# Kernel tuning notes

Hardware: AMD Instinct MI355X
Metric: run time of the kernel (lower is better)

The kernel has to match this reference:

```python
import jax, jax.numpy as jnp
import numpy as np
from jax import lax

N_WIN = 232
T = 8            # timesteps
CHUNK = N_WIN // T  # 29
BETA = 0.9
THR = 1.0
POOL_DIV = 4.0 * 4.0 * 4.0  # avgpool3d kernel volume


@jax.custom_vjp
def spike(x):
    # Heaviside forward (snntorch fire: mem_shift > 0)
    return (x > 0).astype(x.dtype)

def _spike_fwd(x):
    return spike(x), x

def _spike_bwd(x, g):
    # snntorch ATan surrogate, alpha=2: grad = 1 / (1 + (pi*x)^2)
    return (g / (1.0 + (jnp.pi * x) ** 2),)

spike.defvjp(_spike_fwd, _spike_bwd)


def lif(cur, mem, beta, thr):
    # snntorch Leaky, reset_mechanism='subtract': reset uses previous mem
    reset = spike(mem - thr)
    mem_new = beta * mem + cur - reset * thr
    spk = spike(mem_new - thr)
    return spk, mem_new


def setup_inputs() -> dict:
    key = jax.random.key(0)
    ks = jax.random.split(key, 8)
    B, C, H, W = 16, 3, 96, 96
    h0, h1 = 2048, 1024
    input_dim = 47 * 47       # 2209
    in_feat = C * h1 * 13     # 39936
    return {
        "x": jax.random.normal(ks[0], (B, C, N_WIN, H, W), jnp.float32),
        "W_in": jax.random.normal(ks[1], (h0, input_dim), jnp.float32) / np.sqrt(input_dim).astype(np.float32),
        "b_in": jax.random.normal(ks[2], (h0,), jnp.float32) * 0.01,
        "W_hid": jax.random.normal(ks[3], (h1, h0), jnp.float32) / np.sqrt(h0).astype(np.float32),
        "b_hid": jax.random.normal(ks[4], (h1,), jnp.float32) * 0.01,
        "W_out": jax.random.normal(ks[5], (4, in_feat), jnp.float32) / np.sqrt(in_feat).astype(np.float32),
        "b_out": jax.random.normal(ks[6], (4,), jnp.float32) * 0.01,
    }


def reference(x, W_in, b_in, W_hid, b_hid, W_out, b_out):
    B, C, _, H, W = x.shape
    # split time into T chunks of CHUNK, pool each chunk independently
    x6 = x[:, :, : T * CHUNK].reshape(B, C, T, CHUNK, H, W)
    pooled = lax.reduce_window(x6, 0.0, lax.add,
                               (1, 1, 1, 4, 4, 4), (1, 1, 1, 2, 2, 2), "VALID") / POOL_DIV
    Dp, Hp, Wp = pooled.shape[3], pooled.shape[4], pooled.shape[5]  # 13, 47, 47
    # [T, B, C*Dp, Hp*Wp]
    xs = pooled.transpose(2, 0, 1, 3, 4, 5).reshape(T, B, C * Dp, Hp * Wp)
    # fc_in is per-step independent -> precompute for all steps
    cur_in_all = jnp.einsum("tbnf,hf->tbnh", xs, W_in) + b_in

    def step(carry, cur_in):
        m_in, m_hid, m_out = carry
        spk_in, m_in = lif(cur_in, m_in, BETA, THR)
        cur_hid = jnp.einsum("bnh,gh->bng", spk_in, W_hid) + b_hid
        spk_hid, m_hid = lif(cur_hid, m_hid, BETA, THR)
        cur_out = spk_hid.reshape(B, -1) @ W_out.T + b_out
        spk_out, m_out = lif(cur_out, m_out, BETA, 1.0)  # li_out threshold=1.0
        return (m_in, m_hid, m_out), spk_out

    init = (jnp.zeros((B, C * Dp, W_in.shape[0]), x.dtype),
            jnp.zeros((B, C * Dp, W_hid.shape[0]), x.dtype),
            jnp.zeros((B, W_out.shape[0]), x.dtype))
    _, spk_rec = lax.scan(step, init, cur_in_all)
    return spk_rec  # [T, B, n_classes]
```

## Files before the change

### kernel.cpp

```cpp
#include <hip/hip_runtime.h>
#include <hip/hip_bf16.h>

typedef unsigned short ushort_t;
typedef __bf16 bf16x8 __attribute__((ext_vector_type(8)));
typedef float f32x4 __attribute__((ext_vector_type(4)));

#define NROWS 4992
#define KPAD 2240
#define KREAL 2209
#define NH 2048

#define OFF_XS      ((size_t)0)
#define OFF_WINB    ((size_t)22364160)
#define OFF_CURIN   ((size_t)31539200)
#define OFF_CNT1    ((size_t)72433664)
#define OFF_BITS1   ((size_t)72453632)
#define OFF_CNT2    ((size_t)73731584)
#define OFF_BITS2   ((size_t)73732096)
#define ZERO_BYTES  ((size_t)(74371072 - 72433664))
#define OFF_LIST1   ((size_t)74371072)
#define OFF_LIST2   ((size_t)75649024)

#define GLOAD16(g, l) __builtin_amdgcn_global_load_lds( \
    (const __attribute__((address_space(1))) void*)(g), \
    (__attribute__((address_space(3))) void*)(l), 16, 0, 0)

__global__ __launch_bounds__(256) void convert_win(const float* __restrict__ W,
                                                   __hip_bfloat16* __restrict__ Wb) {
    int idx = blockIdx.x * 256 + threadIdx.x;
    int n = idx / KPAD, k = idx - n * KPAD;
    float v = (k < KREAL) ? W[(size_t)n * KREAL + k] : 0.f;
    Wb[idx] = __float2bfloat16(v);
}

__global__ __launch_bounds__(256) void pool_kernel(const float* __restrict__ x,
                                                   __hip_bfloat16* __restrict__ xs) {
    __shared__ float slice[26 * 96];
    __shared__ float acc[2][12 * 47];
    const int tid = threadIdx.x;
    const int band = blockIdx.y;
    const int blk = blockIdx.x;
    const int t = blk & 7;
    const int bc = blk >> 3;
    const int b = bc / 3, c = bc - b * 3;
    const int i0 = band * 12;
    const int ni = (band == 3) ? 11 : 12;
    const int nyf4 = (2 * ni + 2) * 24;
    const int nout = ni * 47;
    const float* xbase = x + ((size_t)bc * 232 + (size_t)t * 29) * 9216 + i0 * 192;

    for (int o = tid; o < nout; o += 256) { acc[0][o] = 0.f; acc[1][o] = 0.f; }

    for (int z = 0; z < 28; ++z) {
        __syncthreads();
        const float4* src = (const float4*)(xbase + (size_t)z * 9216);
        float4* dst = (float4*)slice;
        for (int idx = tid; idx < nyf4; idx += 256) dst[idx] = src[idx];
        __syncthreads();

        const int dmin = (z >= 3) ? ((z - 2) >> 1) : 0;
        int dmax = z >> 1; if (dmax > 12) dmax = 12;
        const bool emit = (z >= 3) && (z & 1);
        const int dem = (z - 3) >> 1;
        const int row = t * 624 + b * 39 + c * 13 + dem;

        for (int o = tid; o < nout; o += 256) {
            int il = o / 47, j = o - il * 47;
            const float* p = slice + (2 * il) * 96 + 2 * j;
            float s = 0.f;
#pragma unroll
            for (int dy = 0; dy < 4; ++dy)
                s += p[dy * 96 + 0] + p[dy * 96 + 1] + p[dy * 96 + 2] + p[dy * 96 + 3];
            for (int d = dmin; d <= dmax; ++d) acc[d & 1][o] += s;
            if (emit) {
                int slot = dem & 1;
                xs[(size_t)row * KPAD + i0 * 47 + o] = __float2bfloat16(acc[slot][o] * 0.015625f);
                acc[slot][o] = 0.f;
            }
        }
        if (emit && band == 0 && tid < KPAD - KREAL) {
            xs[(size_t)row * KPAD + KREAL + tid] = __float2bfloat16(0.f);
        }
    }
}

#define BM 128
#define BN 128
#define BK 32
__global__ __launch_bounds__(256) void gemm_kernel(const ushort_t* __restrict__ A,
                                                   const ushort_t* __restrict__ B,
                                                   float* __restrict__ C) {
    __shared__ ushort_t As[BM * BK];
    __shared__ ushort_t Bs[BN * BK];
    const int tid = threadIdx.x;
    const int m0 = blockIdx.y * BM, n0 = blockIdx.x * BN;
    const int lane = tid & 63, w = tid >> 6;
    const int wm = (w >> 1) * 64, wn = (w & 1) * 64;
    const int lr = lane & 15, quad = lane >> 4;

    f32x4 acc[4][4] = {};

    const int srow = tid >> 2;
    const int sk = (tid & 3) * 8;
    const ushort_t* Ag0 = A + (size_t)(m0 + srow) * KPAD + sk;
    const ushort_t* Ag1 = A + (size_t)(m0 + 64 + srow) * KPAD + sk;
    const ushort_t* Bg0 = B + (size_t)(n0 + srow) * KPAD + sk;
    const ushort_t* Bg1 = B + (size_t)(n0 + 64 + srow) * KPAD + sk;
    ushort_t* Asl0 = &As[srow * BK + sk];
    ushort_t* Asl1 = &As[(64 + srow) * BK + sk];
    ushort_t* Bsl0 = &Bs[srow * BK + sk];
    ushort_t* Bsl1 = &Bs[(64 + srow) * BK + sk];

    for (int k0 = 0; k0 < KPAD; k0 += BK) {
        __syncthreads();
        GLOAD16(Ag0 + k0, Asl0);
        GLOAD16(Ag1 + k0, Asl1);
        GLOAD16(Bg0 + k0, Bsl0);
        GLOAD16(Bg1 + k0, Bsl1);
        __syncthreads();
        bf16x8 af[4], bfr[4];
#pragma unroll
        for (int i = 0; i < 4; ++i)
            af[i] = *(const bf16x8*)&As[(wm + i * 16 + lr) * BK + quad * 8];
#pragma unroll
        for (int j = 0; j < 4; ++j)
            bfr[j] = *(const bf16x8*)&Bs[(wn + j * 16 + lr) * BK + quad * 8];
#pragma unroll
        for (int i = 0; i < 4; ++i)
#pragma unroll
            for (int j = 0; j < 4; ++j)
                acc[i][j] = __builtin_amdgcn_mfma_f32_16x16x32_bf16(af[i], bfr[j], acc[i][j], 0, 0, 0);
    }
#pragma unroll
    for (int i = 0; i < 4; ++i) {
        const int row = m0 + wm + i * 16 + quad * 4;
#pragma unroll
        for (int j = 0; j < 4; ++j) {
            const int col = n0 + wn + j * 16 + lr;
#pragma unroll
            for (int reg = 0; reg < 4; ++reg)
                C[(size_t)(row + reg) * NH + col] = acc[i][j][reg];
        }
    }
}

__global__ __launch_bounds__(256) void lif1_kernel(const float* __restrict__ cur_in,
                                                   const float* __restrict__ b_in,
                                                   int* __restrict__ cnt1,
                                                   int* __restrict__ list1,
                                                   unsigned int* __restrict__ bits1) {
    const int h = blockIdx.x * 256 + threadIdx.x;
    const int row2 = blockIdx.y;
    const float bias = b_in[h];
    float m = 0.f;
#pragma unroll
    for (int t = 0; t < 8; ++t) {
        const int r = t * 624 + row2;
        float cur = cur_in[(size_t)r * NH + h] + bias;
        float reset = (m > 1.f) ? 1.f : 0.f;
        m = 0.9f * m + cur - reset;
        if (m > 1.f) {
            int idx = atomicAdd(&cnt1[r], 1);
            if (idx < 64) list1[r * 64 + idx] = h;
            atomicOr(&bits1[r * 64 + (h >> 5)], 1u << (h & 31));
        }
    }
}

__global__ __launch_bounds__(256) void lif2_kernel(const float* __restrict__ W_hid,
                                                   const float* __restrict__ b_hid,
                                                   const int* __restrict__ cnt1,
                                                   const int* __restrict__ list1,
                                                   const unsigned int* __restrict__ bits1,
                                                   int* __restrict__ cnt2,
                                                   int* __restrict__ list2,
                                                   unsigned int* __restrict__ bits2) {
    const int g = blockIdx.x * 256 + threadIdx.x;
    const int row2 = blockIdx.y;
    const int b = row2 / 39, n = row2 - b * 39;
    const float* Wg = W_hid + (size_t)g * NH;
    const float bias = b_hid[g];
    float m = 0.f;
    for (int t = 0; t < 8; ++t) {
        const int r = t * 624 + row2;
        float cur = bias;
        int c = cnt1[r];
        if (c > 0) {
            if (c <= 64) {
                for (int i2 = 0; i2 < c; ++i2) cur += Wg[list1[r * 64 + i2]];
            } else {
                for (int w2 = 0; w2 < 64; ++w2) {
                    unsigned int v = bits1[r * 64 + w2];
                    while (v) { int h = w2 * 32 + __ffs(v) - 1; v &= v - 1; cur += Wg[h]; }
                }
            }
        }
        float reset = (m > 1.f) ? 1.f : 0.f;
        m = 0.9f * m + cur - reset;
        if (m > 1.f) {
            int rb = t * 16 + b;
            int fidx = n * 1024 + g;
            int idx = atomicAdd(&cnt2[rb], 1);
            if (idx < 256) list2[rb * 256 + idx] = fidx;
            atomicOr(&bits2[rb * 1248 + (fidx >> 5)], 1u << (fidx & 31));
        }
    }
}

__global__ void lif3_kernel(const float* __restrict__ W_out,
                            const float* __restrict__ b_out,
                            const int* __restrict__ cnt2,
                            const int* __restrict__ list2,
                            const unsigned int* __restrict__ bits2,
                            float* __restrict__ out) {
    const int tid = threadIdx.x;
    const int b = tid >> 2, o = tid & 3;
    const float* Wo = W_out + (size_t)o * 39936;
    const float bias = b_out[o];
    float m = 0.f;
    for (int t = 0; t < 8; ++t) {
        const int rb = t * 16 + b;
        float cur = bias;
        int c = cnt2[rb];
        if (c > 0) {
            if (c <= 256) {
                for (int i2 = 0; i2 < c; ++i2) cur += Wo[list2[rb * 256 + i2]];
            } else {
                for (int w2 = 0; w2 < 1248; ++w2) {
                    unsigned int v = bits2[rb * 1248 + w2];
                    while (v) { int f = w2 * 32 + __ffs(v) - 1; v &= v - 1; cur += Wo[f]; }
                }
            }
        }
        float reset = (m > 1.f) ? 1.f : 0.f;
        m = 0.9f * m + cur - reset;
        out[t * 64 + b * 4 + o] = (m > 1.f) ? 1.f : 0.f;
    }
}

extern "C" void kernel_launch(void* const* d_in, const int* in_sizes, int n_in,
                              void* d_out, int out_size, void* d_ws, size_t ws_size,
                              hipStream_t stream) {
    const float* x     = (const float*)d_in[0];
    const float* W_in  = (const float*)d_in[1];
    const float* b_in  = (const float*)d_in[2];
    const float* W_hid = (const float*)d_in[3];
    const float* b_hid = (const float*)d_in[4];
    const float* W_out = (const float*)d_in[5];
    const float* b_out = (const float*)d_in[6];
    float* out = (float*)d_out;
    char* ws = (char*)d_ws;

    __hip_bfloat16* xs_bf  = (__hip_bfloat16*)(ws + OFF_XS);
    __hip_bfloat16* winb   = (__hip_bfloat16*)(ws + OFF_WINB);
    float*          cur_in = (float*)(ws + OFF_CURIN);
    int*            cnt1   = (int*)(ws + OFF_CNT1);
    unsigned int*   bits1  = (unsigned int*)(ws + OFF_BITS1);
    int*            cnt2   = (int*)(ws + OFF_CNT2);
    unsigned int*   bits2  = (unsigned int*)(ws + OFF_BITS2);
    int*            list1  = (int*)(ws + OFF_LIST1);
    int*            list2  = (int*)(ws + OFF_LIST2);

    hipMemsetAsync(ws + OFF_CNT1, 0, ZERO_BYTES, stream);

    convert_win<<<(2048 * KPAD) / 256, 256, 0, stream>>>(W_in, winb);
    pool_kernel<<<dim3(384, 4), 256, 0, stream>>>(x, xs_bf);
    gemm_kernel<<<dim3(NH / BN, NROWS / BM), 256, 0, stream>>>(
        (const ushort_t*)xs_bf, (const ushort_t*)winb, cur_in);
    lif1_kernel<<<dim3(8, 624), 256, 0, stream>>>(cur_in, b_in, cnt1, list1, bits1);
    lif2_kernel<<<dim3(4, 624), 256, 0, stream>>>(W_hid, b_hid, cnt1, list1, bits1,
                                                  cnt2, list2, bits2);
    lif3_kernel<<<1, 64, 0, stream>>>(W_out, b_out, cnt2, list2, bits2, out);
}
```

Before: 700.9 us.

## Fuse first LIF layer into GEMM epilogue via time-interleaved row permutation

Pool output rows are permuted so that each thread's MFMA accumulator fragment holds all 8 timesteps for its (row, hidden) pairs. The GEMM epilogue can then run the first LIF recurrence directly from registers. This removes the 40MB fp32 cur_in write and read-back and drops the separate lif1 launch. The pool kernel also precomputes per-thread output offsets. Atomics now come from the GEMM epilogue, which may serialize more within a block.

```diff
diff --git a/kernel.cpp b/kernel.cpp
--- a/kernel.cpp
+++ b/kernel.cpp
@@ -12,7 +12,6 @@
 
 #define OFF_XS      ((size_t)0)
 #define OFF_WINB    ((size_t)22364160)
-#define OFF_CURIN   ((size_t)31539200)
 #define OFF_CNT1    ((size_t)72433664)
 #define OFF_BITS1   ((size_t)72453632)
 #define OFF_CNT2    ((size_t)73731584)
@@ -24,6 +23,13 @@
 #define GLOAD16(g, l) __builtin_amdgcn_global_load_lds( \
     (const __attribute__((address_space(1))) void*)(g), \
     (__attribute__((address_space(3))) void*)(l), 16, 0, 0)
+
+__device__ __forceinline__ int perm_row(int row2, int t) {
+    const int blkr = row2 >> 4, half = (row2 >> 3) & 1, r8 = row2 & 7;
+    const int q = r8 >> 1, il2 = r8 & 1;
+    const int i_ = il2 | ((t >> 2) << 1), reg = t & 3;
+    return blkr * 128 + half * 64 + i_ * 16 + q * 4 + reg;
+}
 
 __global__ __launch_bounds__(256) void convert_win(const float* __restrict__ W,
                                                    __hip_bfloat16* __restrict__ Wb) {
@@ -49,6 +55,15 @@
     const int nout = ni * 47;
     const float* xbase = x + ((size_t)bc * 232 + (size_t)t * 29) * 9216 + i0 * 192;
 
+    int myo[3], mypo[3];
+    int nmy = 0;
+    for (int o = tid; o < nout; o += 256) {
+        int il = o / 47, j = o - il * 47;
+        myo[nmy] = o;
+        mypo[nmy] = (2 * il) * 96 + 2 * j;
+        ++nmy;
+    }
+
     for (int o = tid; o < nout; o += 256) { acc[0][o] = 0.f; acc[1][o] = 0.f; }
 
     for (int z = 0; z < 28; ++z) {
@@ -62,16 +77,17 @@
         int dmax = z >> 1; if (dmax > 12) dmax = 12;
         const bool emit = (z >= 3) && (z & 1);
         const int dem = (z - 3) >> 1;
-        const int row = t * 624 + b * 39 + c * 13 + dem;
-
-        for (int o = tid; o < nout; o += 256) {
-            int il = o / 47, j = o - il * 47;
-            const float* p = slice + (2 * il) * 96 + 2 * j;
-            float s = 0.f;
+        int row = 0;
+        if (emit) row = perm_row(b * 39 + c * 13 + dem, t);
+
+        for (int s = 0; s < nmy; ++s) {
+            const int o = myo[s];
+            const float* p = slice + mypo[s];
+            float sum = 0.f;
 #pragma unroll
             for (int dy = 0; dy < 4; ++dy)
-                s += p[dy * 96 + 0] + p[dy * 96 + 1] + p[dy * 96 + 2] + p[dy * 96 + 3];
-            for (int d = dmin; d <= dmax; ++d) acc[d & 1][o] += s;
+                sum += p[dy * 96 + 0] + p[dy * 96 + 1] + p[dy * 96 + 2] + p[dy * 96 + 3];
+            for (int d = dmin; d <= dmax; ++d) acc[d & 1][o] += sum;
             if (emit) {
                 int slot = dem & 1;
                 xs[(size_t)row * KPAD + i0 * 47 + o] = __float2bfloat16(acc[slot][o] * 0.015625f);
@@ -87,9 +103,12 @@
 #define BM 128
 #define BN 128
 #define BK 32
-__global__ __launch_bounds__(256) void gemm_kernel(const ushort_t* __restrict__ A,
-                                                   const ushort_t* __restrict__ B,
-                                                   float* __restrict__ C) {
+__global__ __launch_bounds__(256) void gemm_lif1_kernel(const ushort_t* __restrict__ A,
+                                                        const ushort_t* __restrict__ B,
+                                                        const float* __restrict__ b_in,
+                                                        int* __restrict__ cnt1,
+                                                        int* __restrict__ list1,
+                                                        unsigned int* __restrict__ bits1) {
     __shared__ ushort_t As[BM * BK];
     __shared__ ushort_t Bs[BN * BK];
     const int tid = threadIdx.x;
@@ -131,38 +150,28 @@
             for (int j = 0; j < 4; ++j)
                 acc[i][j] = __builtin_amdgcn_mfma_f32_16x16x32_bf16(af[i], bfr[j], acc[i][j], 0, 0, 0);
     }
-#pragma unroll
-    for (int i = 0; i < 4; ++i) {
-        const int row = m0 + wm + i * 16 + quad * 4;
-#pragma unroll
-        for (int j = 0; j < 4; ++j) {
-            const int col = n0 + wn + j * 16 + lr;
-#pragma unroll
-            for (int reg = 0; reg < 4; ++reg)
-                C[(size_t)(row + reg) * NH + col] = acc[i][j][reg];
-        }
-    }
-}
-
-__global__ __launch_bounds__(256) void lif1_kernel(const float* __restrict__ cur_in,
-                                                   const float* __restrict__ b_in,
-                                                   int* __restrict__ cnt1,
-                                                   int* __restrict__ list1,
-                                                   unsigned int* __restrict__ bits1) {
-    const int h = blockIdx.x * 256 + threadIdx.x;
-    const int row2 = blockIdx.y;
-    const float bias = b_in[h];
-    float m = 0.f;
-#pragma unroll
-    for (int t = 0; t < 8; ++t) {
-        const int r = t * 624 + row2;
-        float cur = cur_in[(size_t)r * NH + h] + bias;
-        float reset = (m > 1.f) ? 1.f : 0.f;
-        m = 0.9f * m + cur - reset;
-        if (m > 1.f) {
-            int idx = atomicAdd(&cnt1[r], 1);
-            if (idx < 64) list1[r * 64 + idx] = h;
-            atomicOr(&bits1[r * 64 + (h >> 5)], 1u << (h & 31));
+
+    const int row2_base = blockIdx.y * 16 + (w >> 1) * 8 + quad * 2;
+#pragma unroll
+    for (int j = 0; j < 4; ++j) {
+        const int h = n0 + wn + j * 16 + lr;
+        const float bias = b_in[h];
+#pragma unroll
+        for (int rr = 0; rr < 2; ++rr) {
+            const int r2 = row2_base + rr;
+            float m = 0.f;
+#pragma unroll
+            for (int t = 0; t < 8; ++t) {
+                float cur = acc[rr + 2 * (t >> 2)][j][t & 3] + bias;
+                float reset = (m > 1.f) ? 1.f : 0.f;
+                m = 0.9f * m + cur - reset;
+                if (m > 1.f) {
+                    const int r = t * 624 + r2;
+                    int idx = atomicAdd(&cnt1[r], 1);
+                    if (idx < 64) list1[r * 64 + idx] = h;
+                    atomicOr(&bits1[r * 64 + (h >> 5)], 1u << (h & 31));
+                }
+            }
         }
     }
 }
@@ -253,7 +262,6 @@
 
     __hip_bfloat16* xs_bf  = (__hip_bfloat16*)(ws + OFF_XS);
     __hip_bfloat16* winb   = (__hip_bfloat16*)(ws + OFF_WINB);
-    float*          cur_in = (float*)(ws + OFF_CURIN);
     int*            cnt1   = (int*)(ws + OFF_CNT1);
     unsigned int*   bits1  = (unsigned int*)(ws + OFF_BITS1);
     int*            cnt2   = (int*)(ws + OFF_CNT2);
@@ -265,9 +273,8 @@
 
     convert_win<<<(2048 * KPAD) / 256, 256, 0, stream>>>(W_in, winb);
     pool_kernel<<<dim3(384, 4), 256, 0, stream>>>(x, xs_bf);
-    gemm_kernel<<<dim3(NH / BN, NROWS / BM), 256, 0, stream>>>(
-        (const ushort_t*)xs_bf, (const ushort_t*)winb, cur_in);
-    lif1_kernel<<<dim3(8, 624), 256, 0, stream>>>(cur_in, b_in, cnt1, list1, bits1);
+    gemm_lif1_kernel<<<dim3(NH / BN, NROWS / BM), 256, 0, stream>>>(
+        (const ushort_t*)xs_bf, (const ushort_t*)winb, b_in, cnt1, list1, bits1);
     lif2_kernel<<<dim3(4, 624), 256, 0, stream>>>(W_hid, b_hid, cnt1, list1, bits1,
                                                   cnt2, list2, bits2);
     lif3_kernel<<<1, 64, 0, stream>>>(W_out, b_out, cnt2, list2, bits2, out);
```

New measurement: 651.5 us. 1.08x faster.
